# Optimization experiments

Hardware: AMD Instinct MI355X
Metric: run time of the kernel (lower is better)

The kernel has to match this reference:

```python
import jax, jax.numpy as jnp
import numpy as np

N = 100_000      # nodes
E = 1_600_000    # directed edges
G = 512          # graphs in batch
IN, H, C = 26, 64, 2
EPS = 1e-5       # BatchNorm eps (torch default)


def setup_inputs() -> dict:
    key = jax.random.key(0)
    ks = jax.random.split(key, 12)
    s = 0.1
    return {
        "x": jax.random.normal(ks[0], (N, IN), jnp.float32),
        "edge_row": jax.random.randint(ks[1], (E,), 0, N, jnp.int32),
        "edge_col": jax.random.randint(ks[2], (E,), 0, N, jnp.int32),
        "batch": jnp.sort(jax.random.randint(ks[3], (N,), 0, G, jnp.int32)),
        "W0": jax.random.normal(ks[4], (IN, H), jnp.float32) * s,
        "b0": jnp.zeros((H,), jnp.float32),
        "W1": jax.random.normal(ks[5], (H, H), jnp.float32) * s,
        "b1": jnp.zeros((H,), jnp.float32),
        "W2": jax.random.normal(ks[6], (H, H), jnp.float32) * s,
        "b2": jnp.zeros((H,), jnp.float32),
        "bn_g": jnp.ones((3, H), jnp.float32),
        "bn_b": jnp.zeros((3, H), jnp.float32),
        "bn_m": jnp.zeros((3, H), jnp.float32),
        "bn_v": jnp.ones((3, H), jnp.float32),
        "Wc1": jax.random.normal(ks[7], (2 * H, H), jnp.float32) * s,
        "bc1": jnp.zeros((H,), jnp.float32),
        "Wc2": jax.random.normal(ks[8], (H, C), jnp.float32) * s,
        "bc2": jnp.zeros((C,), jnp.float32),
    }


def reference(x, edge_row, edge_col, batch, W0, b0, W1, b1, W2, b2,
              bn_g, bn_b, bn_m, bn_v, Wc1, bc1, Wc2, bc2):
    n = x.shape[0]
    # GCN normalization with self-loops (PyG gcn_norm)
    sl = jnp.arange(n, dtype=edge_row.dtype)
    row = jnp.concatenate([edge_row, sl])  # sources j
    col = jnp.concatenate([edge_col, sl])  # targets i
    deg = jax.ops.segment_sum(jnp.ones_like(row, jnp.float32), col, num_segments=n)
    dinv = jnp.where(deg > 0, jax.lax.rsqrt(deg), 0.0)
    norm = dinv[row] * dinv[col]  # [E+N]

    def conv(h, W, b):
        h = h @ W                                   # transform first (PyG)
        msg = h[row] * norm[:, None]                # gather + scale
        return jax.ops.segment_sum(msg, col, num_segments=n) + b  # scatter-add

    h = x
    for i, (W, b) in enumerate([(W0, b0), (W1, b1), (W2, b2)]):
        h = conv(h, W, b)
        # BatchNorm (eval: running stats) + ReLU; dropout off at inference
        h = (h - bn_m[i]) * jax.lax.rsqrt(bn_v[i] + EPS) * bn_g[i] + bn_b[i]
        h = jax.nn.relu(h)

    # global mean + max pool over batch vector
    cnt = jax.ops.segment_sum(jnp.ones((n, 1), h.dtype), batch, num_segments=G)
    mean = jax.ops.segment_sum(h, batch, num_segments=G) / jnp.maximum(cnt, 1.0)
    mx = jax.ops.segment_max(h, batch, num_segments=G)
    pooled = jnp.concatenate([mean, mx], axis=1)    # [G, 2H]

    hid = jax.nn.relu(pooled @ Wc1 + bc1)
    return hid @ Wc2 + bc2                          # [G, C]
```

## Files before the change

### kernel.cpp

```cpp
#include <hip/hip_runtime.h>

#define HDIM 64
#define EPSBN 1e-5f
#define MNODES 8
#define CAP 48
#define NB 256
#define BCAP 8192
#define EPB 2048
#define MAXW 400

typedef unsigned short u16;

__device__ __forceinline__ float bf2f(u16 b) {
    return __uint_as_float(((unsigned)b) << 16);
}
__device__ __forceinline__ u16 f2bf_rne(float f) {
    unsigned u = __float_as_uint(f);
    u += 0x7FFFu + ((u >> 16) & 1u);
    return (u16)(u >> 16);
}

__device__ __forceinline__ int bstart_of(int b, int N) {
    return (int)(((long long)b * N + NB - 1) / NB);
}

__global__ __launch_bounds__(256) void bucket_k(
    const int* __restrict__ row, const int* __restrict__ col,
    int* __restrict__ gcnt, int2* __restrict__ bstore, int E, int N,
    const int* __restrict__ batch, int* __restrict__ bounds, int G) {
    __shared__ int hist[NB];
    __shared__ int cur[NB];
    int tid = threadIdx.x;
    hist[tid] = 0;
    for (int i = blockIdx.x * 256 + tid; i < N; i += gridDim.x * 256) {
        int b = batch[i];
        int bp = (i == 0) ? -1 : batch[i - 1];
        for (int g = bp + 1; g <= b; g++) bounds[g] = i;
        if (i == N - 1) { for (int g = b + 1; g <= G; g++) bounds[g] = N; }
    }
    __syncthreads();
    int e0 = blockIdx.x * EPB;
    for (int u = 0; u < EPB / 256; u++) {
        int e = e0 + u * 256 + tid;
        if (e < E) {
            int c = __builtin_nontemporal_load(&col[e]);
            int b = (int)(((unsigned long long)c * NB) / (unsigned)N);
            atomicAdd(&hist[b], 1);
        }
    }
    __syncthreads();
    cur[tid] = atomicAdd(&gcnt[tid], hist[tid]);
    __syncthreads();
    for (int u = 0; u < EPB / 256; u++) {
        int e = e0 + u * 256 + tid;
        if (e < E) {
            int c = __builtin_nontemporal_load(&col[e]);
            int r = __builtin_nontemporal_load(&row[e]);
            int b = (int)(((unsigned long long)c * NB) / (unsigned)N);
            int slot = atomicAdd(&cur[b], 1);
            if (slot < BCAP) bstore[(size_t)b * BCAP + slot] = make_int2(r, c);
        }
    }
}

__global__ __launch_bounds__(256) void csrfill_k(
    const int* __restrict__ gcnt, const int2* __restrict__ bstore,
    int* __restrict__ offs, int* __restrict__ cnt, int* __restrict__ esrc,
    float* __restrict__ dinv, const float* __restrict__ x,
    u16* __restrict__ xp, int INR, int N) {
    __shared__ int lcnt[MAXW];
    __shared__ int lrk[MAXW];
    __shared__ int pref[MAXW];
    __shared__ int sc[256];
    int b = blockIdx.x, tid = threadIdx.x;
    int bs = bstart_of(b, N);
    int be = bstart_of(b + 1, N);
    int width = be - bs;

    int gv = min(gcnt[tid], BCAP);
    sc[tid] = gv;
    __syncthreads();
    for (int o = 1; o < 256; o <<= 1) {
        int t2 = (tid >= o) ? sc[tid - o] : 0;
        __syncthreads();
        sc[tid] += t2;
        __syncthreads();
    }
    int base = (b == 0) ? 0 : sc[b - 1];

    for (int t = tid; t < width; t += 256) { lcnt[t] = 0; lrk[t] = 0; }
    __syncthreads();
    int M = min(gcnt[b], BCAP);
    const int2* bsp = bstore + (size_t)b * BCAP;
    for (int k = tid; k < M; k += 256) atomicAdd(&lcnt[bsp[k].y - bs], 1);
    __syncthreads();
    int c0 = (2 * tid     < width) ? min(lcnt[2 * tid],     CAP) : 0;
    int c1 = (2 * tid + 1 < width) ? min(lcnt[2 * tid + 1], CAP) : 0;
    sc[tid] = c0 + c1;
    __syncthreads();
    for (int o = 1; o < 256; o <<= 1) {
        int t2 = (tid >= o) ? sc[tid - o] : 0;
        __syncthreads();
        sc[tid] += t2;
        __syncthreads();
    }
    int pairExcl = sc[tid] - (c0 + c1);
    if (2 * tid     < width) pref[2 * tid]     = pairExcl;
    if (2 * tid + 1 < width) pref[2 * tid + 1] = pairExcl + c0;
    __syncthreads();
    for (int t = tid; t < width; t += 256) {
        offs[bs + t] = base + pref[t];
        cnt[bs + t] = min(lcnt[t], CAP);
    }
    for (int idx = tid; idx < width * 32; idx += 256) {
        int tl = idx >> 5, k = idx & 31;
        int i = bs + tl;
        float di = rsqrtf((float)min(lcnt[tl], CAP) + 1.0f);
        if (k == 0) dinv[i] = di;
        float xv = (k < INR) ? __builtin_nontemporal_load(&x[i * INR + k]) : 0.f;
        xp[i * 32 + k] = f2bf_rne(di * xv);
    }
    for (int k = tid; k < M; k += 256) {
        int2 rc = bsp[k];
        int l = rc.y - bs;
        int rank = atomicAdd(&lrk[l], 1);
        if (rank < CAP) esrc[base + pref[l] + rank] = rc.x;
    }
}

template <int KIN, bool SCALEOUT>
__global__ __launch_bounds__(64) void conv_k(
    const u16* __restrict__ hb, const int* __restrict__ offs,
    const int* __restrict__ cnt, const int* __restrict__ esrc,
    const float* __restrict__ dinv,
    const float* __restrict__ W, int KINR,
    const float* __restrict__ bias, const float* __restrict__ g,
    const float* __restrict__ bb, const float* __restrict__ m,
    const float* __restrict__ v, void* __restrict__ hout_, int n) {
    int lane = threadIdx.x;
    float wreg[KIN];
#pragma unroll
    for (int k = 0; k < KIN; k++) wreg[k] = (k < KINR) ? W[k * HDIM + lane] : 0.f;
    const float sc = g[lane] * rsqrtf(v[lane] + EPSBN);
    const float sh = (bias[lane] - m[lane]) * sc + bb[lane];

    __shared__ float agg4[4][KIN];

    const int feat = lane & (KIN - 1);
    auto ldh = [&](int node) -> float {
        return bf2f(hb[(size_t)node * KIN + feat]);
    };

    for (int grp = 0; grp < 2; grp++) {
        int ibase = blockIdx.x * MNODES + grp * 4;
        if (ibase >= n) break;
        float acc0 = 0.f, acc1 = 0.f, acc2 = 0.f, acc3 = 0.f;
        int e0 = 0, n0 = 0, e1 = 0, n1 = 0, e2 = 0, n2 = 0, e3 = 0, n3 = 0;
        {
            acc0 = ldh(ibase); e0 = offs[ibase]; n0 = e0 + cnt[ibase];
            if (ibase + 1 < n) { acc1 = ldh(ibase + 1); e1 = offs[ibase + 1]; n1 = e1 + cnt[ibase + 1]; }
            if (ibase + 2 < n) { acc2 = ldh(ibase + 2); e2 = offs[ibase + 2]; n2 = e2 + cnt[ibase + 2]; }
            if (ibase + 3 < n) { acc3 = ldh(ibase + 3); e3 = offs[ibase + 3]; n3 = e3 + cnt[ibase + 3]; }
        }
        while (e0 + 2 <= n0 && e1 + 2 <= n1 && e2 + 2 <= n2 && e3 + 2 <= n3) {
            int s00 = esrc[e0], s01 = esrc[e0 + 1];
            int s10 = esrc[e1], s11 = esrc[e1 + 1];
            int s20 = esrc[e2], s21 = esrc[e2 + 1];
            int s30 = esrc[e3], s31 = esrc[e3 + 1];
            float h00 = ldh(s00), h01 = ldh(s01);
            float h10 = ldh(s10), h11 = ldh(s11);
            float h20 = ldh(s20), h21 = ldh(s21);
            float h30 = ldh(s30), h31 = ldh(s31);
            acc0 += h00 + h01;
            acc1 += h10 + h11;
            acc2 += h20 + h21;
            acc3 += h30 + h31;
            e0 += 2; e1 += 2; e2 += 2; e3 += 2;
        }
#define DRAIN(ek, nk, ak)                                                     \
        for (; ek + 4 <= nk; ek += 4) {                                       \
            int a = esrc[ek], b = esrc[ek + 1], c = esrc[ek + 2], d = esrc[ek + 3]; \
            float ha = ldh(a), hb2 = ldh(b), hc = ldh(c), hd = ldh(d);        \
            ak += (ha + hb2) + (hc + hd);                                     \
        }                                                                     \
        for (; ek < nk; ek++) ak += ldh(esrc[ek]);
        DRAIN(e0, n0, acc0)
        DRAIN(e1, n1, acc1)
        DRAIN(e2, n2, acc2)
        DRAIN(e3, n3, acc3)
#undef DRAIN

        __syncthreads();
        if (lane < KIN) {
            agg4[0][lane] = acc0; agg4[1][lane] = acc1;
            agg4[2][lane] = acc2; agg4[3][lane] = acc3;
        }
        __syncthreads();
        for (int q = 0; q < 4; q++) {
            int i = ibase + q;
            if (i >= n) break;
            float di = dinv[i];
            float dot = 0.f;
            const float4* aggv = (const float4*)agg4[q];
#pragma unroll
            for (int k4 = 0; k4 < KIN / 4; k4++) {
                float4 a = aggv[k4];
                dot = fmaf(a.x, wreg[4 * k4 + 0], dot);
                dot = fmaf(a.y, wreg[4 * k4 + 1], dot);
                dot = fmaf(a.z, wreg[4 * k4 + 2], dot);
                dot = fmaf(a.w, wreg[4 * k4 + 3], dot);
            }
            float y = fmaxf(fmaf(dot * di, sc, sh), 0.f);
            if (SCALEOUT) ((u16*)hout_)[(size_t)i * HDIM + lane] = f2bf_rne(di * y);
            else          ((float*)hout_)[(size_t)i * HDIM + lane] = y;
        }
    }
}

__global__ __launch_bounds__(256) void pool_mlp_k(
    const float* __restrict__ h, const int* __restrict__ bounds,
    const float* __restrict__ Wc1, const float* __restrict__ bc1,
    const float* __restrict__ Wc2, const float* __restrict__ bc2,
    float* __restrict__ out, int n) {
    int gidx = blockIdx.x;
    int tid = threadIdx.x;
    int lane = tid & 63;
    int wv = tid >> 6;

    int start = bounds[gidx], end = bounds[gidx + 1];

    float sum = 0.f, mx = 0.f;
    for (int i = start + wv; i < end; i += 4) {
        float val = h[(size_t)i * HDIM + lane];
        sum += val;
        mx = fmaxf(mx, val);
    }
    __shared__ float ssum[4 * HDIM];
    __shared__ float smax[4 * HDIM];
    __shared__ float pooled[2 * HDIM];
    ssum[wv * HDIM + lane] = sum;
    smax[wv * HDIM + lane] = mx;
    __syncthreads();
    if (wv == 0) {
        float sv = ssum[lane] + ssum[64 + lane] + ssum[128 + lane] + ssum[192 + lane];
        float mm = fmaxf(fmaxf(smax[lane], smax[64 + lane]),
                         fmaxf(smax[128 + lane], smax[192 + lane]));
        int cntg = end - start;
        pooled[lane] = sv / fmaxf((float)cntg, 1.f);
        pooled[HDIM + lane] = mm;
    }
    __syncthreads();
    if (wv == 0) {
        float a = bc1[lane];
#pragma unroll
        for (int k = 0; k < 2 * HDIM; k++) a = fmaf(pooled[k], Wc1[k * HDIM + lane], a);
        a = fmaxf(a, 0.f);
#pragma unroll
        for (int c = 0; c < 2; c++) {
            float vv = a * Wc2[lane * 2 + c];
            for (int off = 32; off; off >>= 1) vv += __shfl_down(vv, off);
            if (lane == 0) out[gidx * 2 + c] = vv + bc2[c];
        }
    }
}

extern "C" void kernel_launch(void* const* d_in, const int* in_sizes, int n_in,
                              void* d_out, int out_size, void* d_ws, size_t ws_size,
                              hipStream_t stream) {
    const float* x    = (const float*)d_in[0];
    const int*   erow = (const int*)d_in[1];
    const int*   ecol = (const int*)d_in[2];
    const int*   batch= (const int*)d_in[3];
    const float* W0   = (const float*)d_in[4];
    const float* b0   = (const float*)d_in[5];
    const float* W1   = (const float*)d_in[6];
    const float* b1   = (const float*)d_in[7];
    const float* W2   = (const float*)d_in[8];
    const float* b2   = (const float*)d_in[9];
    const float* bn_g = (const float*)d_in[10];
    const float* bn_b = (const float*)d_in[11];
    const float* bn_m = (const float*)d_in[12];
    const float* bn_v = (const float*)d_in[13];
    const float* Wc1  = (const float*)d_in[14];
    const float* bc1  = (const float*)d_in[15];
    const float* Wc2  = (const float*)d_in[16];
    const float* bc2  = (const float*)d_in[17];
    float* out = (float*)d_out;

    const int N = in_sizes[3];
    const int E = in_sizes[1];
    const int G = out_size / 2;
    const int INR = in_sizes[0] / N;

    char* ws = (char*)d_ws;
    size_t off = 0;
    auto alloc = [&](size_t bytes) -> void* {
        void* p = ws + off;
        off += (bytes + 255) & ~(size_t)255;
        return p;
    };
    int*   gcnt   = (int*)alloc(NB * 4);
    int*   offs   = (int*)alloc((size_t)N * 4);
    int*   cnt    = (int*)alloc((size_t)N * 4);
    float* dinv   = (float*)alloc((size_t)N * 4);
    int*   bounds = (int*)alloc((size_t)(512 + 1) * 4);
    int2*  bstore = (int2*)alloc((size_t)NB * BCAP * 8);
    int*   esrc   = (int*)alloc((size_t)E * 4 + 256);
    void*  bufA   = alloc((size_t)N * HDIM * 4);
    void*  bufB   = alloc((size_t)N * HDIM * 4);
    (void)ws_size;

    hipMemsetAsync(gcnt, 0, NB * 4, stream);
    int nbk = (E + EPB - 1) / EPB;
    bucket_k<<<nbk, 256, 0, stream>>>(erow, ecol, gcnt, bstore, E, N, batch, bounds, G);
    csrfill_k<<<NB, 256, 0, stream>>>(gcnt, bstore, offs, cnt, esrc, dinv, x, (u16*)bufB, INR, N);

    int cgrid = (N + MNODES - 1) / MNODES;
    conv_k<32, true><<<cgrid, 64, 0, stream>>>((const u16*)bufB, offs, cnt, esrc, dinv, W0, INR, b0,
        bn_g + 0, bn_b + 0, bn_m + 0, bn_v + 0, bufA, N);
    conv_k<64, true><<<cgrid, 64, 0, stream>>>((const u16*)bufA, offs, cnt, esrc, dinv, W1, 64, b1,
        bn_g + 64, bn_b + 64, bn_m + 64, bn_v + 64, bufB, N);
    conv_k<64, false><<<cgrid, 64, 0, stream>>>((const u16*)bufB, offs, cnt, esrc, dinv, W2, 64, b2,
        bn_g + 128, bn_b + 128, bn_m + 128, bn_v + 128, bufA, N);

    pool_mlp_k<<<G, 256, 0, stream>>>((const float*)bufA, bounds, Wc1, bc1, Wc2, bc2, out, N);
}
```

Measured before the change: 386.5 us.

## Split wavefront lanes across edges with packed bf16 pair loads in conv gather

The conv gather now has each lane load a 32-bit pair of bf16 features, so one wavefront covers several edges at once (64/(KIN/2) edges per step) instead of every lane reading one feature of a single edge. Partial sums are combined across edge slots with xor shuffles before the dense transform. This is meant to use the lanes that previously sat idle or did duplicate reads when KIN < 64, and to cut the number of serial gather steps per node. In exchange it adds a per-lane select over the loaded source indices, masking for partial groups, and a shuffle reduction.

New measurement: 471.3 us. 21.9% more time.

```diff
diff --git a/kernel.cpp b/kernel.cpp
--- a/kernel.cpp
+++ b/kernel.cpp
@@ -10,6 +10,7 @@
 #define MAXW 400
 
 typedef unsigned short u16;
+typedef unsigned int u32;
 
 __device__ __forceinline__ float bf2f(u16 b) {
     return __uint_as_float(((unsigned)b) << 16);
@@ -19,6 +20,8 @@
     u += 0x7FFFu + ((u >> 16) & 1u);
     return (u16)(u >> 16);
 }
+__device__ __forceinline__ float lo16f(u32 u) { return __uint_as_float(u << 16); }
+__device__ __forceinline__ float hi16f(u32 u) { return __uint_as_float(u & 0xFFFF0000u); }
 
 __device__ __forceinline__ int bstart_of(int b, int N) {
     return (int)(((long long)b * N + NB - 1) / NB);
@@ -137,7 +140,13 @@
     const float* __restrict__ bias, const float* __restrict__ g,
     const float* __restrict__ bb, const float* __restrict__ m,
     const float* __restrict__ v, void* __restrict__ hout_, int n) {
+    constexpr int LPR = KIN / 2;
+    constexpr int EPI = 64 / LPR;
+    const u32* hp = (const u32*)hb;
     int lane = threadIdx.x;
+    const int fp = lane & (LPR - 1);
+    const int slot = lane / LPR;
+
     float wreg[KIN];
 #pragma unroll
     for (int k = 0; k < KIN; k++) wreg[k] = (k < KINR) ? W[k * HDIM + lane] : 0.f;
@@ -146,54 +155,65 @@
 
     __shared__ float agg4[4][KIN];
 
-    const int feat = lane & (KIN - 1);
-    auto ldh = [&](int node) -> float {
-        return bf2f(hb[(size_t)node * KIN + feat]);
+    auto ldpair = [&](int node) -> u32 {
+        return hp[(size_t)node * LPR + fp];
     };
+
+#define GROUP(ek, nk, ik, a0, a1)                                              \
+    {                                                                          \
+        int sv[EPI];                                                           \
+        _Pragma("unroll")                                                      \
+        for (int t = 0; t < EPI; t++) sv[t] = esrc[ek + t];        \
+        int src = sv[0];                                                       \
+        _Pragma("unroll")                                                      \
+        for (int t = 1; t < EPI; t++) src = (slot == t) ? sv[t] : src;         \
+        bool valid = (ek + slot) < nk;                                         \
+        src = valid ? src : ik;                                                \
+        u32 u = ldpair(src);                                                   \
+        a0 += valid ? lo16f(u) : 0.f;                                          \
+        a1 += valid ? hi16f(u) : 0.f;                                          \
+        ek += EPI;                                                             \
+    }
 
     for (int grp = 0; grp < 2; grp++) {
         int ibase = blockIdx.x * MNODES + grp * 4;
         if (ibase >= n) break;
-        float acc0 = 0.f, acc1 = 0.f, acc2 = 0.f, acc3 = 0.f;
-        int e0 = 0, n0 = 0, e1 = 0, n1 = 0, e2 = 0, n2 = 0, e3 = 0, n3 = 0;
-        {
-            acc0 = ldh(ibase); e0 = offs[ibase]; n0 = e0 + cnt[ibase];
-            if (ibase + 1 < n) { acc1 = ldh(ibase + 1); e1 = offs[ibase + 1]; n1 = e1 + cnt[ibase + 1]; }
-            if (ibase + 2 < n) { acc2 = ldh(ibase + 2); e2 = offs[ibase + 2]; n2 = e2 + cnt[ibase + 2]; }
-            if (ibase + 3 < n) { acc3 = ldh(ibase + 3); e3 = offs[ibase + 3]; n3 = e3 + cnt[ibase + 3]; }
-        }
-        while (e0 + 2 <= n0 && e1 + 2 <= n1 && e2 + 2 <= n2 && e3 + 2 <= n3) {
-            int s00 = esrc[e0], s01 = esrc[e0 + 1];
-            int s10 = esrc[e1], s11 = esrc[e1 + 1];
-            int s20 = esrc[e2], s21 = esrc[e2 + 1];
-            int s30 = esrc[e3], s31 = esrc[e3 + 1];
-            float h00 = ldh(s00), h01 = ldh(s01);
-            float h10 = ldh(s10), h11 = ldh(s11);
-            float h20 = ldh(s20), h21 = ldh(s21);
-            float h30 = ldh(s30), h31 = ldh(s31);
-            acc0 += h00 + h01;
-            acc1 += h10 + h11;
-            acc2 += h20 + h21;
-            acc3 += h30 + h31;
-            e0 += 2; e1 += 2; e2 += 2; e3 += 2;
-        }
-#define DRAIN(ek, nk, ak)                                                     \
-        for (; ek + 4 <= nk; ek += 4) {                                       \
-            int a = esrc[ek], b = esrc[ek + 1], c = esrc[ek + 2], d = esrc[ek + 3]; \
-            float ha = ldh(a), hb2 = ldh(b), hc = ldh(c), hd = ldh(d);        \
-            ak += (ha + hb2) + (hc + hd);                                     \
-        }                                                                     \
-        for (; ek < nk; ek++) ak += ldh(esrc[ek]);
-        DRAIN(e0, n0, acc0)
-        DRAIN(e1, n1, acc1)
-        DRAIN(e2, n2, acc2)
-        DRAIN(e3, n3, acc3)
-#undef DRAIN
-
-        __syncthreads();
-        if (lane < KIN) {
-            agg4[0][lane] = acc0; agg4[1][lane] = acc1;
-            agg4[2][lane] = acc2; agg4[3][lane] = acc3;
+        int i0n = ibase, i1n = min(ibase + 1, n - 1),
+            i2n = min(ibase + 2, n - 1), i3n = min(ibase + 3, n - 1);
+        float a00 = 0.f, a01 = 0.f, a10 = 0.f, a11 = 0.f;
+        float a20 = 0.f, a21 = 0.f, a30 = 0.f, a31 = 0.f;
+        int e0 = offs[i0n], n0 = e0 + cnt[i0n];
+        int e1 = offs[i1n], n1 = e1 + cnt[i1n];
+        int e2 = offs[i2n], n2 = e2 + cnt[i2n];
+        int e3 = offs[i3n], n3 = e3 + cnt[i3n];
+        if (ibase + 1 >= n) { n1 = e1; }
+        if (ibase + 2 >= n) { n2 = e2; }
+        if (ibase + 3 >= n) { n3 = e3; }
+
+        while (e0 < n0 || e1 < n1 || e2 < n2 || e3 < n3) {
+            if (e0 < n0) GROUP(e0, n0, i0n, a00, a01)
+            if (e1 < n1) GROUP(e1, n1, i1n, a10, a11)
+            if (e2 < n2) GROUP(e2, n2, i2n, a20, a21)
+            if (e3 < n3) GROUP(e3, n3, i3n, a30, a31)
+        }
+#pragma unroll
+        for (int o = LPR; o < 64; o <<= 1) {
+            a00 += __shfl_xor(a00, o); a01 += __shfl_xor(a01, o);
+            a10 += __shfl_xor(a10, o); a11 += __shfl_xor(a11, o);
+            a20 += __shfl_xor(a20, o); a21 += __shfl_xor(a21, o);
+            a30 += __shfl_xor(a30, o); a31 += __shfl_xor(a31, o);
+        }
+        { u32 u = ldpair(i0n); a00 += lo16f(u); a01 += hi16f(u); }
+        if (ibase + 1 < n) { u32 u = ldpair(i1n); a10 += lo16f(u); a11 += hi16f(u); }
+        if (ibase + 2 < n) { u32 u = ldpair(i2n); a20 += lo16f(u); a21 += hi16f(u); }
+        if (ibase + 3 < n) { u32 u = ldpair(i3n); a30 += lo16f(u); a31 += hi16f(u); }
+
+        __syncthreads();
+        if (slot == 0) {
+            *(float2*)&agg4[0][2 * fp] = make_float2(a00, a01);
+            *(float2*)&agg4[1][2 * fp] = make_float2(a10, a11);
+            *(float2*)&agg4[2][2 * fp] = make_float2(a20, a21);
+            *(float2*)&agg4[3][2 * fp] = make_float2(a30, a31);
         }
         __syncthreads();
         for (int q = 0; q < 4; q++) {
@@ -215,6 +235,7 @@
             else          ((float*)hout_)[(size_t)i * HDIM + lane] = y;
         }
     }
+#undef GROUP
 }
 
 __global__ __launch_bounds__(256) void pool_mlp_k(
```
